# Performance work log

Measured on AMD Instinct MI355X. Metric: run time of the kernel, lower is better.

Reference implementation:

```python
import jax, jax.numpy as jnp
import numpy as np

NUM_HEADS = 16


def _rope(x_BHLd, freqs_cis):
    # x: [B,H,L,d], freqs_cis: [L, d//2, 2] (cos, sin)
    B, H, L, d = x_BHLd.shape
    xs = x_BHLd.reshape(B, H, L, d // 2, 2)
    fc = freqs_cis.reshape(1, 1, L, d // 2, 2)
    real = xs[..., 0] * fc[..., 0] - xs[..., 1] * fc[..., 1]
    imag = xs[..., 1] * fc[..., 0] + xs[..., 0] * fc[..., 1]
    return jnp.stack([real, imag], axis=-1).reshape(B, H, L, d)


def setup_inputs() -> dict:
    key = jax.random.key(0)
    k1, k2 = jax.random.split(key)
    B, L, D = 1, 4096, 1024
    d = D // NUM_HEADS
    x = jax.random.normal(k1, (B, L, D), dtype=jnp.float32)
    Wqkv = jax.random.normal(k2, (D, 3 * D), dtype=jnp.float32) * (D ** -0.5)
    bqkv = jnp.zeros((3 * D,), dtype=jnp.float32)
    # true rotary cos/sin table: [L, d//2, 2]
    base = 10000.0
    inv_freq = 1.0 / (base ** (jnp.arange(0, d, 2, dtype=jnp.float32) / d))  # [d//2]
    t = jnp.arange(L, dtype=jnp.float32)
    ang = jnp.outer(t, inv_freq)  # [L, d//2]
    freqs_cis = jnp.stack([jnp.cos(ang), jnp.sin(ang)], axis=-1)  # [L, d//2, 2]
    return {"x": x, "freqs_cis": freqs_cis, "Wqkv": Wqkv, "bqkv": bqkv}


def reference(x, freqs_cis, Wqkv, bqkv):
    B, L, D = x.shape
    H = NUM_HEADS
    d = D // H
    qkv = x @ Wqkv + bqkv  # [B,L,3D]
    q, k, v = jnp.split(qkv, 3, axis=-1)
    split = lambda t: t.reshape(B, L, H, d).transpose(0, 2, 1, 3)  # [B,H,L,d]
    q, k, v = split(q), split(k), split(v)
    q = _rope(q, freqs_cis)
    k = _rope(k, freqs_cis)
    scale = 1.0 / jnp.sqrt(jnp.asarray(d, dtype=q.dtype))
    scores = jnp.einsum('bhqd,bhkd->bhqk', q, k) * scale  # [B,H,L,L]
    causal = jnp.tril(jnp.ones((L, L), dtype=bool))
    scores = jnp.where(causal, scores, jnp.asarray(-jnp.inf, dtype=scores.dtype))
    probs = jax.nn.softmax(scores, axis=-1)
    out = jnp.einsum('bhqk,bhkd->bhqd', probs, v)  # [B,H,L,d]
    return out.transpose(0, 2, 1, 3).reshape(B, L, D)
```

## Files before the change

### kernel.cpp

```cpp
#include <hip/hip_runtime.h>

typedef short short8 __attribute__((ext_vector_type(8)));
typedef float f32x4 __attribute__((ext_vector_type(4)));
typedef unsigned short u16;
typedef unsigned short u16x4 __attribute__((ext_vector_type(4)));
typedef unsigned short u16x8 __attribute__((ext_vector_type(8)));

#define L_SEQ 4096
#define NHEAD 16
#define HDIM  64
#define DMODEL 1024
#define N3    3072
#define HL    (L_SEQ * HDIM)

__device__ __forceinline__ u16 f2bf(float f) {
  union { float f; unsigned u; } v; v.f = f;
  return (u16)((v.u + 0x7fffu + ((v.u >> 16) & 1u)) >> 16);
}

__device__ __forceinline__ unsigned cvt_pk_bf16(float lo, float hi) {
  unsigned r;
  asm("v_cvt_pk_bf16_f32 %0, %1, %2" : "=v"(r) : "v"(lo), "v"(hi));
  return r;
}

__device__ __forceinline__ void gl2lds16(const void* g, void* l) {
  __builtin_amdgcn_global_load_lds(
      (const __attribute__((address_space(1))) unsigned int*)g,
      (__attribute__((address_space(3))) unsigned int*)l, 16, 0, 0);
}

__device__ __forceinline__ float fexp2(float x) { return __builtin_amdgcn_exp2f(x); }

__global__ void cvt_fused_kernel(const float* __restrict__ x, u16* __restrict__ xb,
                                 const float* __restrict__ W, u16* __restrict__ Wt) {
  if (blockIdx.x < 2048) {
    int i = blockIdx.x * blockDim.x + threadIdx.x;
    const f32x4* p = (const f32x4*)x + (size_t)i * 2;
    f32x4 a = p[0], b = p[1];
    u16x8 o;
    o[0] = f2bf(a[0]); o[1] = f2bf(a[1]); o[2] = f2bf(a[2]); o[3] = f2bf(a[3]);
    o[4] = f2bf(b[0]); o[5] = f2bf(b[1]); o[6] = f2bf(b[2]); o[7] = f2bf(b[3]);
    ((u16x8*)xb)[i] = o;
  } else {
    __shared__ float t[64][65];
    int idx = blockIdx.x - 2048;
    int k0 = (idx & 15) * 64, n0 = (idx >> 4) * 64;
    int tr = threadIdx.x >> 4;
    int tc = (threadIdx.x & 15) * 4;
    for (int rr = tr; rr < 64; rr += 16) {
      f32x4 v = *(const f32x4*)&W[(size_t)(k0 + rr) * N3 + n0 + tc];
      t[rr][tc] = v[0]; t[rr][tc + 1] = v[1]; t[rr][tc + 2] = v[2]; t[rr][tc + 3] = v[3];
    }
    __syncthreads();
    for (int rr = tr; rr < 64; rr += 16) {
      u16x4 o;
      o[0] = f2bf(t[tc + 0][rr]); o[1] = f2bf(t[tc + 1][rr]);
      o[2] = f2bf(t[tc + 2][rr]); o[3] = f2bf(t[tc + 3][rr]);
      *(u16x4*)&Wt[(size_t)(n0 + rr) * DMODEL + k0 + tc] = o;
    }
  }
}

#define GBM 128
#define GBN 128
#define GBK 64

__global__ __launch_bounds__(256, 2) void gemm_qkv_kernel(
    const u16* __restrict__ xb, const u16* __restrict__ wt,
    const float* __restrict__ bias, const float* __restrict__ freqs,
    u16* __restrict__ Qb, u16* __restrict__ Kb, u16* __restrict__ Vt) {
  __shared__ u16 Asm[GBM * GBK];
  __shared__ u16 Bsm[GBN * GBK];
  const int tid = threadIdx.x, lane = tid & 63, wid = tid >> 6;
  const int lr = lane & 15, lh = lane >> 4;
  const int swz = (blockIdx.x % 8) * 96 + blockIdx.x / 8;
  const int bx = swz % (N3 / GBN), by = swz / (N3 / GBN);
  const int m0 = by * GBM, n0 = bx * GBN;
  const int wr = wid >> 1, wc = wid & 1;
  const char* xbB = (const char*)xb;
  const char* wtB = (const char*)wt;
  char* AsmB = (char*)Asm;
  char* BsmB = (char*)Bsm;

  int pbase[4]; size_t srcAoff[4], srcBoff[4];
#pragma unroll
  for (int i = 0; i < 4; i++) {
    int p = wid * 4096 + i * 1024 + lane * 16;
    int row = p >> 7, slot = (p & 127) >> 4;
    int sw = (slot ^ (row & 7)) * 16;
    pbase[i] = p;
    srcAoff[i] = (size_t)(m0 + row) * (DMODEL * 2) + sw;
    srcBoff[i] = (size_t)(n0 + row) * (DMODEL * 2) + sw;
  }

  int aoff[4][2], boff[4][2];
#pragma unroll
  for (int mi = 0; mi < 4; mi++) {
    int row = wr * 64 + mi * 16 + lr;
#pragma unroll
    for (int kc = 0; kc < 2; kc++)
      aoff[mi][kc] = row * 128 + ((kc * 64 + lh * 16) ^ ((row & 7) << 4));
  }
#pragma unroll
  for (int ni = 0; ni < 4; ni++) {
    int row = wc * 64 + ni * 16 + lr;
#pragma unroll
    for (int kc = 0; kc < 2; kc++)
      boff[ni][kc] = row * 128 + ((kc * 64 + lh * 16) ^ ((row & 7) << 4));
  }

  f32x4 acc[4][4] = {};

  for (int k0 = 0; k0 < DMODEL; k0 += GBK) {
    __syncthreads();
#pragma unroll
    for (int i = 0; i < 4; i++) {
      gl2lds16(xbB + srcAoff[i] + (size_t)k0 * 2, AsmB + pbase[i]);
      gl2lds16(wtB + srcBoff[i] + (size_t)k0 * 2, BsmB + pbase[i]);
    }
    __syncthreads();
#pragma unroll
    for (int kc = 0; kc < 2; kc++) {
      short8 a[4], b[4];
#pragma unroll
      for (int mi = 0; mi < 4; mi++) a[mi] = *(const short8*)(AsmB + aoff[mi][kc]);
#pragma unroll
      for (int ni = 0; ni < 4; ni++) b[ni] = *(const short8*)(BsmB + boff[ni][kc]);
#pragma unroll
      for (int mi = 0; mi < 4; mi++)
#pragma unroll
        for (int ni = 0; ni < 4; ni++)
          acc[mi][ni] = __builtin_amdgcn_mfma_f32_16x16x32_bf16(a[mi], b[ni], acc[mi][ni], 0, 0, 0);
    }
  }

  const float QSCALE = 0.125f * 1.44269504088896f;
  const int colbase = n0 + wc * 64;
#pragma unroll
  for (int ni = 0; ni < 4; ni++) {
    int col = colbase + ni * 16 + lr;
    float bv = bias[col];
    int sect = col >> 10;
    int cc = col & 1023;
    int h = cc >> 6, j = cc & 63;
#pragma unroll
    for (int mi = 0; mi < 4; mi++) {
      int row0 = m0 + wr * 64 + mi * 16 + lh * 4;
      float v[4];
#pragma unroll
      for (int r = 0; r < 4; r++) v[r] = acc[mi][ni][r] + bv;
      if (sect < 2) {
        int i2 = j >> 1;
        bool odd = (j & 1) != 0;
#pragma unroll
        for (int r = 0; r < 4; r++) {
          float pv = __shfl_xor(v[r], 1);
          float2 cs = *(const float2*)&freqs[((size_t)(row0 + r) * 32 + i2) * 2];
          v[r] = odd ? (v[r] * cs.x + pv * cs.y) : (v[r] * cs.x - pv * cs.y);
          if (sect == 0) v[r] *= QSCALE;
        }
        u16* dst = (sect == 0 ? Qb : Kb) + (size_t)h * HL + (size_t)row0 * HDIM + j;
#pragma unroll
        for (int r = 0; r < 4; r++) dst[(size_t)r * HDIM] = f2bf(v[r]);
      } else {
        u16x4 o;
#pragma unroll
        for (int r = 0; r < 4; r++) o[r] = f2bf(v[r]);
        *(u16x4*)&Vt[(size_t)h * HL + (size_t)j * L_SEQ + row0] = o;
      }
    }
  }
}

#define QBLK 64
#define KBLK 64

__global__ __launch_bounds__(256, 4) void flash_kernel(
    const u16* __restrict__ Qb, const u16* __restrict__ Kb,
    const u16* __restrict__ Vt, float* __restrict__ out) {
  __shared__ char Ksm[2][KBLK * 128];
  __shared__ char Vsm[2][HDIM * KBLK * 2];
  __shared__ char Psm[4][16 * 128];
  const int tid = threadIdx.x, lane = tid & 63, wid = tid >> 6;
  const int lr = lane & 15, lh = lane >> 4;
  const int bid = blockIdx.x;
  const int h = bid & 15;
  const int pr = bid >> 4;
  const char* Qh = (const char*)(Qb + (size_t)h * HL);
  const char* Kh = (const char*)(Kb + (size_t)h * HL);
  const char* Vh = (const char*)(Vt + (size_t)h * HL);
  char* Pw = Psm[wid];

  int pOff[2], KsrcOff[2], VsrcOff[2];
#pragma unroll
  for (int i = 0; i < 2; i++) {
    int p = wid * 2048 + i * 1024 + lane * 16;
    int row = p >> 7, slot = (p & 127) >> 4;
    int sw = (slot ^ (row & 7)) << 4;
    pOff[i] = p;
    KsrcOff[i] = row * 128 + sw;
    VsrcOff[i] = row * (L_SEQ * 2) + sw;
  }

  for (int pass = 0; pass < 2; ++pass) {
    const int qb = pass == 0 ? (63 - pr) : pr;
    const int q0 = qb * QBLK;
    const int wmin = q0 + wid * 16;
    const int qrow = wmin + lr;
    const int nt = qb + 1;

    short8 qa[2];
    {
      int row = q0 + wid * 16 + lr;
#pragma unroll
      for (int kc = 0; kc < 2; kc++)
        qa[kc] = *(const short8*)(Qh + (size_t)row * 128 + kc * 64 + lh * 16);
    }

    f32x4 o[4] = {};
    float m_r = -__builtin_inff(), ls = 0.f;

#pragma unroll
    for (int i = 0; i < 2; i++) {
      gl2lds16(Kh + KsrcOff[i], Ksm[0] + pOff[i]);
      gl2lds16(Vh + VsrcOff[i], Vsm[0] + pOff[i]);
    }
    __syncthreads();

    for (int t = 0; t < nt; ++t) {
      const int kt = t * KBLK;
      const int cur = t & 1;
      if (t + 1 < nt) {
        const size_t kn128 = (size_t)(kt + KBLK) * 128;
        const size_t kn2 = (size_t)(kt + KBLK) * 2;
#pragma unroll
        for (int i = 0; i < 2; i++) {
          gl2lds16(Kh + kn128 + KsrcOff[i], Ksm[cur ^ 1] + pOff[i]);
          gl2lds16(Vh + kn2 + VsrcOff[i], Vsm[cur ^ 1] + pOff[i]);
        }
      }
      const char* Kc = Ksm[cur];
      const char* Vc = Vsm[cur];

      f32x4 sfr[4];
      __builtin_amdgcn_s_setprio(1);
#pragma unroll
      for (int ni = 0; ni < 4; ni++) {
        int row = ni * 16 + lr;
        short8 bk0 = *(const short8*)(Kc + row * 128 + ((lh * 16) ^ ((row & 7) << 4)));
        short8 bk1 = *(const short8*)(Kc + row * 128 + ((64 + lh * 16) ^ ((row & 7) << 4)));
        f32x4 z = {};
        z = __builtin_amdgcn_mfma_f32_16x16x32_bf16(bk0, qa[0], z, 0, 0, 0);
        z = __builtin_amdgcn_mfma_f32_16x16x32_bf16(bk1, qa[1], z, 0, 0, 0);
        sfr[ni] = z;
      }
      __builtin_amdgcn_s_setprio(0);

      if (kt + KBLK - 1 > wmin) {
#pragma unroll
        for (int ni = 0; ni < 4; ni++)
#pragma unroll
          for (int r = 0; r < 4; r++)
            if (kt + ni * 16 + lh * 4 + r > qrow) sfr[ni][r] = -__builtin_inff();
      }

      float pmax = sfr[0][0];
#pragma unroll
      for (int ni = 0; ni < 4; ni++)
#pragma unroll
        for (int r = 0; r < 4; r++) pmax = fmaxf(pmax, sfr[ni][r]);
      pmax = fmaxf(pmax, __shfl_xor(pmax, 16));
      pmax = fmaxf(pmax, __shfl_xor(pmax, 32));

      if (__any(pmax > m_r + 8.f)) {
        float mn = fmaxf(m_r, pmax);
        float alpha = fexp2(m_r - mn);
        m_r = mn;
        ls *= alpha;
        float ao[4];
#pragma unroll
        for (int r = 0; r < 4; r++) ao[r] = __shfl(alpha, (lane & 48) | (lh * 4 + r));
#pragma unroll
        for (int vn = 0; vn < 4; vn++)
#pragma unroll
          for (int r = 0; r < 4; r++) o[vn][r] *= ao[r];
      }

      float psum = 0.f;
      unsigned Wp[4][2];
#pragma unroll
      for (int ni = 0; ni < 4; ni++) {
        float p0 = fexp2(sfr[ni][0] - m_r);
        float p1 = fexp2(sfr[ni][1] - m_r);
        float p2 = fexp2(sfr[ni][2] - m_r);
        float p3 = fexp2(sfr[ni][3] - m_r);
        psum += (p0 + p1) + (p2 + p3);
        Wp[ni][0] = cvt_pk_bf16(p0, p1);
        Wp[ni][1] = cvt_pk_bf16(p2, p3);
      }
      ls += psum;

#pragma unroll
      for (int ni = 0; ni < 4; ni++) {
        uint2 w2; w2.x = Wp[ni][0]; w2.y = Wp[ni][1];
        *(uint2*)(Pw + lr * 128 + ((ni * 32 + lh * 8) ^ ((lr & 7) << 4))) = w2;
      }
      asm volatile("s_waitcnt lgkmcnt(0)" ::: "memory");

      __builtin_amdgcn_s_setprio(1);
#pragma unroll
      for (int pc = 0; pc < 2; pc++) {
        short8 pa = *(const short8*)(Pw + lr * 128 + ((pc * 64 + lh * 16) ^ ((lr & 7) << 4)));
#pragma unroll
        for (int vn = 0; vn < 4; vn++) {
          int vrow = vn * 16 + lr;
          short8 bv = *(const short8*)(Vc + vrow * 128 + ((pc * 64 + lh * 16) ^ ((vrow & 7) << 4)));
          o[vn] = __builtin_amdgcn_mfma_f32_16x16x32_bf16(pa, bv, o[vn], 0, 0, 0);
        }
      }
      __builtin_amdgcn_s_setprio(0);

      __syncthreads();
    }

    ls += __shfl_xor(ls, 16);
    ls += __shfl_xor(ls, 32);
    float inv = 1.0f / ls;
    float invo[4];
#pragma unroll
    for (int r = 0; r < 4; r++) invo[r] = __shfl(inv, (lane & 48) | (lh * 4 + r));
#pragma unroll
    for (int r = 0; r < 4; r++) {
      int rowv = wmin + lh * 4 + r;
      float* op = out + (size_t)rowv * DMODEL + h * HDIM;
#pragma unroll
      for (int vn = 0; vn < 4; vn++) op[vn * 16 + lr] = o[vn][r] * invo[r];
    }
  }
}

extern "C" void kernel_launch(void* const* d_in, const int* in_sizes, int n_in,
                              void* d_out, int out_size, void* d_ws, size_t ws_size,
                              hipStream_t stream) {
  const float* x = (const float*)d_in[0];
  const float* freqs = (const float*)d_in[1];
  const float* W = (const float*)d_in[2];
  const float* bias = (const float*)d_in[3];
  float* out = (float*)d_out;

  char* ws = (char*)d_ws;
  u16* xb = (u16*)ws;
  u16* wt = (u16*)(ws + 8u * 1024 * 1024);
  u16* Qb = (u16*)(ws + 14u * 1024 * 1024);
  u16* Kb = (u16*)(ws + 22u * 1024 * 1024);
  u16* Vt = (u16*)(ws + 30u * 1024 * 1024);

  cvt_fused_kernel<<<2816, 256, 0, stream>>>(x, xb, W, wt);
  gemm_qkv_kernel<<<768, 256, 0, stream>>>(xb, wt, bias, freqs, Qb, Kb, Vt);
  flash_kernel<<<512, 256, 0, stream>>>(Qb, Kb, Vt, out);
}
```

Before: 129.4 us.

## Switch flash attention to 32x32 MFMA tiles with 128-row query blocks

```diff
diff --git a/kernel.cpp b/kernel.cpp
--- a/kernel.cpp
+++ b/kernel.cpp
@@ -2,6 +2,7 @@
 
 typedef short short8 __attribute__((ext_vector_type(8)));
 typedef float f32x4 __attribute__((ext_vector_type(4)));
+typedef float f32x16 __attribute__((ext_vector_type(16)));
 typedef unsigned short u16;
 typedef unsigned short u16x4 __attribute__((ext_vector_type(4)));
 typedef unsigned short u16x8 __attribute__((ext_vector_type(8)));
@@ -173,24 +174,34 @@
   }
 }
 
-#define QBLK 64
+#define QBLK 128
 #define KBLK 64
-
-__global__ __launch_bounds__(256, 4) void flash_kernel(
+#define LD8(p) (*(const short8*)(p))
+
+__global__ __launch_bounds__(256, 2) void flash_kernel(
     const u16* __restrict__ Qb, const u16* __restrict__ Kb,
     const u16* __restrict__ Vt, float* __restrict__ out) {
   __shared__ char Ksm[2][KBLK * 128];
   __shared__ char Vsm[2][HDIM * KBLK * 2];
-  __shared__ char Psm[4][16 * 128];
   const int tid = threadIdx.x, lane = tid & 63, wid = tid >> 6;
-  const int lr = lane & 15, lh = lane >> 4;
+  const int l31 = lane & 31, hf = lane >> 5;
   const int bid = blockIdx.x;
   const int h = bid & 15;
-  const int pr = bid >> 4;
+  const int qt = 31 - (bid >> 4);
+  const int q0 = qt * QBLK;
+  const int q0w = q0 + wid * 32;
+  const int qrow = q0w + l31;
   const char* Qh = (const char*)(Qb + (size_t)h * HL);
   const char* Kh = (const char*)(Kb + (size_t)h * HL);
   const char* Vh = (const char*)(Vt + (size_t)h * HL);
-  char* Pw = Psm[wid];
+
+  short8 qa[4];
+#pragma unroll
+  for (int ds = 0; ds < 4; ds++)
+    qa[ds] = LD8(Qh + (size_t)qrow * 128 + ds * 32 + hf * 16);
+
+  f32x16 o0 = {}, o1 = {};
+  float m_r = -__builtin_inff(), ls = 0.f;
 
   int pOff[2], KsrcOff[2], VsrcOff[2];
 #pragma unroll
@@ -203,74 +214,73 @@
     VsrcOff[i] = row * (L_SEQ * 2) + sw;
   }
 
-  for (int pass = 0; pass < 2; ++pass) {
-    const int qb = pass == 0 ? (63 - pr) : pr;
-    const int q0 = qb * QBLK;
-    const int wmin = q0 + wid * 16;
-    const int qrow = wmin + lr;
-    const int nt = qb + 1;
-
-    short8 qa[2];
-    {
-      int row = q0 + wid * 16 + lr;
-#pragma unroll
-      for (int kc = 0; kc < 2; kc++)
-        qa[kc] = *(const short8*)(Qh + (size_t)row * 128 + kc * 64 + lh * 16);
-    }
-
-    f32x4 o[4] = {};
-    float m_r = -__builtin_inff(), ls = 0.f;
-
-#pragma unroll
-    for (int i = 0; i < 2; i++) {
-      gl2lds16(Kh + KsrcOff[i], Ksm[0] + pOff[i]);
-      gl2lds16(Vh + VsrcOff[i], Vsm[0] + pOff[i]);
-    }
-    __syncthreads();
-
-    for (int t = 0; t < nt; ++t) {
-      const int kt = t * KBLK;
-      const int cur = t & 1;
-      if (t + 1 < nt) {
-        const size_t kn128 = (size_t)(kt + KBLK) * 128;
-        const size_t kn2 = (size_t)(kt + KBLK) * 2;
-#pragma unroll
-        for (int i = 0; i < 2; i++) {
-          gl2lds16(Kh + kn128 + KsrcOff[i], Ksm[cur ^ 1] + pOff[i]);
-          gl2lds16(Vh + kn2 + VsrcOff[i], Vsm[cur ^ 1] + pOff[i]);
+  const int nt = 2 * qt + 2;
+
+#pragma unroll
+  for (int i = 0; i < 2; i++) {
+    gl2lds16(Kh + KsrcOff[i], Ksm[0] + pOff[i]);
+    gl2lds16(Vh + VsrcOff[i], Vsm[0] + pOff[i]);
+  }
+  __syncthreads();
+
+  for (int t = 0; t < nt; ++t) {
+    const int kt = t * KBLK;
+    const int cur = t & 1;
+    if (t + 1 < nt) {
+      const size_t kn128 = (size_t)(kt + KBLK) * 128;
+      const size_t kn2 = (size_t)(kt + KBLK) * 2;
+#pragma unroll
+      for (int i = 0; i < 2; i++) {
+        gl2lds16(Kh + kn128 + KsrcOff[i], Ksm[cur ^ 1] + pOff[i]);
+        gl2lds16(Vh + kn2 + VsrcOff[i], Vsm[cur ^ 1] + pOff[i]);
+      }
+    }
+    const char* Kc = Ksm[cur];
+    const char* Vc = Vsm[cur];
+
+    if (kt <= q0w + 31) {
+      const bool do1 = (kt + 32) <= (q0w + 31);
+
+      f32x16 s0 = {}, s1 = {};
+      __builtin_amdgcn_s_setprio(1);
+#pragma unroll
+      for (int ds = 0; ds < 4; ds++) {
+        int off = (ds * 32 + hf * 16);
+        short8 k0 = LD8(Kc + l31 * 128 + (off ^ ((l31 & 7) << 4)));
+        s0 = __builtin_amdgcn_mfma_f32_32x32x16_bf16(k0, qa[ds], s0, 0, 0, 0);
+      }
+      if (do1) {
+#pragma unroll
+        for (int ds = 0; ds < 4; ds++) {
+          int off = (ds * 32 + hf * 16);
+          short8 k1 = LD8(Kc + (32 + l31) * 128 + (off ^ (((32 + l31) & 7) << 4)));
+          s1 = __builtin_amdgcn_mfma_f32_32x32x16_bf16(k1, qa[ds], s1, 0, 0, 0);
         }
       }
-      const char* Kc = Ksm[cur];
-      const char* Vc = Vsm[cur];
-
-      f32x4 sfr[4];
-      __builtin_amdgcn_s_setprio(1);
-#pragma unroll
-      for (int ni = 0; ni < 4; ni++) {
-        int row = ni * 16 + lr;
-        short8 bk0 = *(const short8*)(Kc + row * 128 + ((lh * 16) ^ ((row & 7) << 4)));
-        short8 bk1 = *(const short8*)(Kc + row * 128 + ((64 + lh * 16) ^ ((row & 7) << 4)));
-        f32x4 z = {};
-        z = __builtin_amdgcn_mfma_f32_16x16x32_bf16(bk0, qa[0], z, 0, 0, 0);
-        z = __builtin_amdgcn_mfma_f32_16x16x32_bf16(bk1, qa[1], z, 0, 0, 0);
-        sfr[ni] = z;
-      }
       __builtin_amdgcn_s_setprio(0);
 
-      if (kt + KBLK - 1 > wmin) {
-#pragma unroll
-        for (int ni = 0; ni < 4; ni++)
-#pragma unroll
-          for (int r = 0; r < 4; r++)
-            if (kt + ni * 16 + lh * 4 + r > qrow) sfr[ni][r] = -__builtin_inff();
-      }
-
-      float pmax = sfr[0][0];
-#pragma unroll
-      for (int ni = 0; ni < 4; ni++)
-#pragma unroll
-        for (int r = 0; r < 4; r++) pmax = fmaxf(pmax, sfr[ni][r]);
-      pmax = fmaxf(pmax, __shfl_xor(pmax, 16));
+      if (kt + 31 > q0w) {
+#pragma unroll
+        for (int r = 0; r < 16; r++) {
+          int kl = (r & 3) + 8 * (r >> 2) + 4 * hf;
+          if (kt + kl > qrow) s0[r] = -__builtin_inff();
+        }
+      }
+      if (do1 && (kt + 63 > q0w)) {
+#pragma unroll
+        for (int r = 0; r < 16; r++) {
+          int kl = (r & 3) + 8 * (r >> 2) + 4 * hf;
+          if (kt + 32 + kl > qrow) s1[r] = -__builtin_inff();
+        }
+      }
+
+      float pmax = s0[0];
+#pragma unroll
+      for (int r = 1; r < 16; r++) pmax = fmaxf(pmax, s0[r]);
+      if (do1) {
+#pragma unroll
+        for (int r = 0; r < 16; r++) pmax = fmaxf(pmax, s1[r]);
+      }
       pmax = fmaxf(pmax, __shfl_xor(pmax, 32));
 
       if (__any(pmax > m_r + 8.f)) {
@@ -278,65 +288,67 @@
         float alpha = fexp2(m_r - mn);
         m_r = mn;
         ls *= alpha;
-        float ao[4];
-#pragma unroll
-        for (int r = 0; r < 4; r++) ao[r] = __shfl(alpha, (lane & 48) | (lh * 4 + r));
-#pragma unroll
-        for (int vn = 0; vn < 4; vn++)
-#pragma unroll
-          for (int r = 0; r < 4; r++) o[vn][r] *= ao[r];
-      }
-
-      float psum = 0.f;
-      unsigned Wp[4][2];
-#pragma unroll
-      for (int ni = 0; ni < 4; ni++) {
-        float p0 = fexp2(sfr[ni][0] - m_r);
-        float p1 = fexp2(sfr[ni][1] - m_r);
-        float p2 = fexp2(sfr[ni][2] - m_r);
-        float p3 = fexp2(sfr[ni][3] - m_r);
-        psum += (p0 + p1) + (p2 + p3);
-        Wp[ni][0] = cvt_pk_bf16(p0, p1);
-        Wp[ni][1] = cvt_pk_bf16(p2, p3);
-      }
-      ls += psum;
-
-#pragma unroll
-      for (int ni = 0; ni < 4; ni++) {
-        uint2 w2; w2.x = Wp[ni][0]; w2.y = Wp[ni][1];
-        *(uint2*)(Pw + lr * 128 + ((ni * 32 + lh * 8) ^ ((lr & 7) << 4))) = w2;
-      }
-      asm volatile("s_waitcnt lgkmcnt(0)" ::: "memory");
-
-      __builtin_amdgcn_s_setprio(1);
-#pragma unroll
-      for (int pc = 0; pc < 2; pc++) {
-        short8 pa = *(const short8*)(Pw + lr * 128 + ((pc * 64 + lh * 16) ^ ((lr & 7) << 4)));
-#pragma unroll
-        for (int vn = 0; vn < 4; vn++) {
-          int vrow = vn * 16 + lr;
-          short8 bv = *(const short8*)(Vc + vrow * 128 + ((pc * 64 + lh * 16) ^ ((vrow & 7) << 4)));
-          o[vn] = __builtin_amdgcn_mfma_f32_16x16x32_bf16(pa, bv, o[vn], 0, 0, 0);
-        }
-      }
-      __builtin_amdgcn_s_setprio(0);
-
-      __syncthreads();
-    }
-
-    ls += __shfl_xor(ls, 16);
-    ls += __shfl_xor(ls, 32);
-    float inv = 1.0f / ls;
-    float invo[4];
-#pragma unroll
-    for (int r = 0; r < 4; r++) invo[r] = __shfl(inv, (lane & 48) | (lh * 4 + r));
-#pragma unroll
-    for (int r = 0; r < 4; r++) {
-      int rowv = wmin + lh * 4 + r;
-      float* op = out + (size_t)rowv * DMODEL + h * HDIM;
-#pragma unroll
-      for (int vn = 0; vn < 4; vn++) op[vn * 16 + lr] = o[vn][r] * invo[r];
-    }
+        float ao[16];
+#pragma unroll
+        for (int r = 0; r < 16; r++)
+          ao[r] = __shfl(alpha, (r & 3) + 8 * (r >> 2) + 4 * hf);
+#pragma unroll
+        for (int r = 0; r < 16; r++) { o0[r] *= ao[r]; o1[r] *= ao[r]; }
+      }
+
+#define KST_BLOCK(SREG, KST)                                                      \
+      {                                                                           \
+        float e[16]; float ps = 0.f;                                              \
+        _Pragma("unroll")                                                         \
+        for (int r = 0; r < 16; r++) { e[r] = fexp2(SREG[r] - m_r); ps += e[r]; } \
+        ls += ps;                                                                 \
+        unsigned pk[8];                                                           \
+        _Pragma("unroll")                                                         \
+        for (int m = 0; m < 8; m++) pk[m] = cvt_pk_bf16(e[2 * m], e[2 * m + 1]);  \
+        unsigned x0 = __shfl_xor(hf ? pk[0] : pk[2], 32);                         \
+        unsigned x1 = __shfl_xor(hf ? pk[1] : pk[3], 32);                         \
+        unsigned x2 = __shfl_xor(hf ? pk[4] : pk[6], 32);                         \
+        unsigned x3 = __shfl_xor(hf ? pk[5] : pk[7], 32);                         \
+        union { unsigned u[4]; short8 s8; } A0, A1;                               \
+        A0.u[0] = hf ? x0 : pk[0]; A0.u[1] = hf ? x1 : pk[1];                     \
+        A0.u[2] = hf ? pk[2] : x0; A0.u[3] = hf ? pk[3] : x1;                     \
+        A1.u[0] = hf ? x2 : pk[4]; A1.u[1] = hf ? x3 : pk[5];                     \
+        A1.u[2] = hf ? pk[6] : x2; A1.u[3] = hf ? pk[7] : x3;                     \
+        __builtin_amdgcn_s_setprio(1);                                            \
+        {                                                                         \
+          int vr0 = l31, vr1 = 32 + l31;                                          \
+          short8 v00 = LD8(Vc + vr0 * 128 + (((KST) * 64 + hf * 16) ^ ((vr0 & 7) << 4)));      \
+          short8 v01 = LD8(Vc + vr0 * 128 + (((KST) * 64 + 32 + hf * 16) ^ ((vr0 & 7) << 4))); \
+          o0 = __builtin_amdgcn_mfma_f32_32x32x16_bf16(A0.s8, v00, o0, 0, 0, 0);  \
+          o0 = __builtin_amdgcn_mfma_f32_32x32x16_bf16(A1.s8, v01, o0, 0, 0, 0);  \
+          short8 v10 = LD8(Vc + vr1 * 128 + (((KST) * 64 + hf * 16) ^ ((vr1 & 7) << 4)));      \
+          short8 v11 = LD8(Vc + vr1 * 128 + (((KST) * 64 + 32 + hf * 16) ^ ((vr1 & 7) << 4))); \
+          o1 = __builtin_amdgcn_mfma_f32_32x32x16_bf16(A0.s8, v10, o1, 0, 0, 0);  \
+          o1 = __builtin_amdgcn_mfma_f32_32x32x16_bf16(A1.s8, v11, o1, 0, 0, 0);  \
+        }                                                                         \
+        __builtin_amdgcn_s_setprio(0);                                            \
+      }
+
+      KST_BLOCK(s0, 0)
+      if (do1) KST_BLOCK(s1, 1)
+#undef KST_BLOCK
+    }
+
+    __syncthreads();
+  }
+
+  ls += __shfl_xor(ls, 32);
+  float inv = 1.0f / ls;
+  float invo[16];
+#pragma unroll
+  for (int r = 0; r < 16; r++)
+    invo[r] = __shfl(inv, (r & 3) + 8 * (r >> 2) + 4 * hf);
+#pragma unroll
+  for (int r = 0; r < 16; r++) {
+    int rowq = q0w + (r & 3) + 8 * (r >> 2) + 4 * hf;
+    float* op = out + (size_t)rowq * DMODEL + h * HDIM;
+    op[l31] = o0[r] * invo[r];
+    op[32 + l31] = o1[r] * invo[r];
   }
 }
 
```

After: 145.0 us. 12.0% more time.

## Use 128-row query tiles with 8 waves sharing each K/V tile

Applied to the files above, without the earlier changes.

```diff
diff --git a/kernel.cpp b/kernel.cpp
--- a/kernel.cpp
+++ b/kernel.cpp
@@ -173,76 +173,65 @@
   }
 }
 
-#define QBLK 64
+#define QBLK 128
 #define KBLK 64
 
-__global__ __launch_bounds__(256, 4) void flash_kernel(
+__global__ __launch_bounds__(512, 2) void flash_kernel(
     const u16* __restrict__ Qb, const u16* __restrict__ Kb,
     const u16* __restrict__ Vt, float* __restrict__ out) {
   __shared__ char Ksm[2][KBLK * 128];
   __shared__ char Vsm[2][HDIM * KBLK * 2];
-  __shared__ char Psm[4][16 * 128];
+  __shared__ char Psm[8][16 * 128];
   const int tid = threadIdx.x, lane = tid & 63, wid = tid >> 6;
   const int lr = lane & 15, lh = lane >> 4;
   const int bid = blockIdx.x;
   const int h = bid & 15;
-  const int pr = bid >> 4;
+  const int s = bid >> 4;
+  const int qt = (s < 16) ? s : (47 - s);
+  const int q0 = qt * QBLK;
   const char* Qh = (const char*)(Qb + (size_t)h * HL);
   const char* Kh = (const char*)(Kb + (size_t)h * HL);
   const char* Vh = (const char*)(Vt + (size_t)h * HL);
+
+  const int wmin = q0 + wid * 16;
+  const int qrow = wmin + lr;
   char* Pw = Psm[wid];
 
-  int pOff[2], KsrcOff[2], VsrcOff[2];
-#pragma unroll
-  for (int i = 0; i < 2; i++) {
-    int p = wid * 2048 + i * 1024 + lane * 16;
+  short8 qa[2];
+#pragma unroll
+  for (int kc = 0; kc < 2; kc++)
+    qa[kc] = *(const short8*)(Qh + (size_t)qrow * 128 + kc * 64 + lh * 16);
+
+  f32x4 o[4] = {};
+  float m_r = -__builtin_inff(), ls = 0.f;
+
+  int pOff, KsrcOff, VsrcOff;
+  {
+    int p = wid * 1024 + lane * 16;
     int row = p >> 7, slot = (p & 127) >> 4;
     int sw = (slot ^ (row & 7)) << 4;
-    pOff[i] = p;
-    KsrcOff[i] = row * 128 + sw;
-    VsrcOff[i] = row * (L_SEQ * 2) + sw;
-  }
-
-  for (int pass = 0; pass < 2; ++pass) {
-    const int qb = pass == 0 ? (63 - pr) : pr;
-    const int q0 = qb * QBLK;
-    const int wmin = q0 + wid * 16;
-    const int qrow = wmin + lr;
-    const int nt = qb + 1;
-
-    short8 qa[2];
-    {
-      int row = q0 + wid * 16 + lr;
-#pragma unroll
-      for (int kc = 0; kc < 2; kc++)
-        qa[kc] = *(const short8*)(Qh + (size_t)row * 128 + kc * 64 + lh * 16);
-    }
-
-    f32x4 o[4] = {};
-    float m_r = -__builtin_inff(), ls = 0.f;
-
-#pragma unroll
-    for (int i = 0; i < 2; i++) {
-      gl2lds16(Kh + KsrcOff[i], Ksm[0] + pOff[i]);
-      gl2lds16(Vh + VsrcOff[i], Vsm[0] + pOff[i]);
-    }
-    __syncthreads();
-
-    for (int t = 0; t < nt; ++t) {
-      const int kt = t * KBLK;
-      const int cur = t & 1;
-      if (t + 1 < nt) {
-        const size_t kn128 = (size_t)(kt + KBLK) * 128;
-        const size_t kn2 = (size_t)(kt + KBLK) * 2;
-#pragma unroll
-        for (int i = 0; i < 2; i++) {
-          gl2lds16(Kh + kn128 + KsrcOff[i], Ksm[cur ^ 1] + pOff[i]);
-          gl2lds16(Vh + kn2 + VsrcOff[i], Vsm[cur ^ 1] + pOff[i]);
-        }
-      }
-      const char* Kc = Ksm[cur];
-      const char* Vc = Vsm[cur];
-
+    pOff = p;
+    KsrcOff = row * 128 + sw;
+    VsrcOff = row * (L_SEQ * 2) + sw;
+  }
+
+  const int nt = 2 * qt + 2;
+
+  gl2lds16(Kh + KsrcOff, Ksm[0] + pOff);
+  gl2lds16(Vh + VsrcOff, Vsm[0] + pOff);
+  __syncthreads();
+
+  for (int t = 0; t < nt; ++t) {
+    const int kt = t * KBLK;
+    const int cur = t & 1;
+    if (t + 1 < nt) {
+      gl2lds16(Kh + (size_t)(kt + KBLK) * 128 + KsrcOff, Ksm[cur ^ 1] + pOff);
+      gl2lds16(Vh + (size_t)(kt + KBLK) * 2 + VsrcOff, Vsm[cur ^ 1] + pOff);
+    }
+    const char* Kc = Ksm[cur];
+    const char* Vc = Vsm[cur];
+
+    if (kt <= wmin + 15) {
       f32x4 sfr[4];
       __builtin_amdgcn_s_setprio(1);
 #pragma unroll
@@ -320,23 +309,23 @@
         }
       }
       __builtin_amdgcn_s_setprio(0);
-
-      __syncthreads();
-    }
-
-    ls += __shfl_xor(ls, 16);
-    ls += __shfl_xor(ls, 32);
-    float inv = 1.0f / ls;
-    float invo[4];
-#pragma unroll
-    for (int r = 0; r < 4; r++) invo[r] = __shfl(inv, (lane & 48) | (lh * 4 + r));
-#pragma unroll
-    for (int r = 0; r < 4; r++) {
-      int rowv = wmin + lh * 4 + r;
-      float* op = out + (size_t)rowv * DMODEL + h * HDIM;
-#pragma unroll
-      for (int vn = 0; vn < 4; vn++) op[vn * 16 + lr] = o[vn][r] * invo[r];
-    }
+    }
+
+    __syncthreads();
+  }
+
+  ls += __shfl_xor(ls, 16);
+  ls += __shfl_xor(ls, 32);
+  float inv = 1.0f / ls;
+  float invo[4];
+#pragma unroll
+  for (int r = 0; r < 4; r++) invo[r] = __shfl(inv, (lane & 48) | (lh * 4 + r));
+#pragma unroll
+  for (int r = 0; r < 4; r++) {
+    int rowv = wmin + lh * 4 + r;
+    float* op = out + (size_t)rowv * DMODEL + h * HDIM;
+#pragma unroll
+    for (int vn = 0; vn < 4; vn++) op[vn * 16 + lr] = o[vn][r] * invo[r];
   }
 }
 
@@ -358,5 +347,5 @@
 
   cvt_fused_kernel<<<2816, 256, 0, stream>>>(x, xb, W, wt);
   gemm_qkv_kernel<<<768, 256, 0, stream>>>(xb, wt, bias, freqs, Qb, Kb, Vt);
-  flash_kernel<<<512, 256, 0, stream>>>(Qb, Kb, Vt, out);
-}
+  flash_kernel<<<512, 512, 0, stream>>>(Qb, Kb, Vt, out);
+}
```

Result: slower. 135.5 us (+4.7%).

## Double KV tile to 128 keys and skip fully masked causal sub-tiles

Applied to the files above, without the earlier changes.

```diff
diff --git a/kernel.cpp b/kernel.cpp
--- a/kernel.cpp
+++ b/kernel.cpp
@@ -174,14 +174,14 @@
 }
 
 #define QBLK 64
-#define KBLK 64
-
-__global__ __launch_bounds__(256, 4) void flash_kernel(
+#define KBLK 128
+
+__global__ __launch_bounds__(256, 2) void flash_kernel(
     const u16* __restrict__ Qb, const u16* __restrict__ Kb,
     const u16* __restrict__ Vt, float* __restrict__ out) {
   __shared__ char Ksm[2][KBLK * 128];
   __shared__ char Vsm[2][HDIM * KBLK * 2];
-  __shared__ char Psm[4][16 * 128];
+  __shared__ char Psm[4][16 * 256];
   const int tid = threadIdx.x, lane = tid & 63, wid = tid >> 6;
   const int lr = lane & 15, lh = lane >> 4;
   const int bid = blockIdx.x;
@@ -192,15 +192,19 @@
   const char* Vh = (const char*)(Vt + (size_t)h * HL);
   char* Pw = Psm[wid];
 
-  int pOff[2], KsrcOff[2], VsrcOff[2];
-#pragma unroll
-  for (int i = 0; i < 2; i++) {
-    int p = wid * 2048 + i * 1024 + lane * 16;
-    int row = p >> 7, slot = (p & 127) >> 4;
-    int sw = (slot ^ (row & 7)) << 4;
+  int pOff[4], KsrcOff[4], VsrcOff[4];
+#pragma unroll
+  for (int i = 0; i < 4; i++) {
+    int p = wid * 4096 + i * 1024 + lane * 16;
+    {
+      int row = p >> 7, slot = (p & 127) >> 4;
+      KsrcOff[i] = row * 128 + ((slot ^ (row & 7)) << 4);
+    }
+    {
+      int row = p >> 8, slot = (p & 255) >> 4;
+      VsrcOff[i] = row * (L_SEQ * 2) + ((slot ^ (row & 7)) << 4);
+    }
     pOff[i] = p;
-    KsrcOff[i] = row * 128 + sw;
-    VsrcOff[i] = row * (L_SEQ * 2) + sw;
   }
 
   for (int pass = 0; pass < 2; ++pass) {
@@ -208,21 +212,18 @@
     const int q0 = qb * QBLK;
     const int wmin = q0 + wid * 16;
     const int qrow = wmin + lr;
-    const int nt = qb + 1;
+    const int nt = qb / 2 + 1;
 
     short8 qa[2];
-    {
-      int row = q0 + wid * 16 + lr;
-#pragma unroll
-      for (int kc = 0; kc < 2; kc++)
-        qa[kc] = *(const short8*)(Qh + (size_t)row * 128 + kc * 64 + lh * 16);
-    }
+#pragma unroll
+    for (int kc = 0; kc < 2; kc++)
+      qa[kc] = *(const short8*)(Qh + (size_t)qrow * 128 + kc * 64 + lh * 16);
 
     f32x4 o[4] = {};
     float m_r = -__builtin_inff(), ls = 0.f;
 
 #pragma unroll
-    for (int i = 0; i < 2; i++) {
+    for (int i = 0; i < 4; i++) {
       gl2lds16(Kh + KsrcOff[i], Ksm[0] + pOff[i]);
       gl2lds16(Vh + VsrcOff[i], Vsm[0] + pOff[i]);
     }
@@ -235,41 +236,44 @@
         const size_t kn128 = (size_t)(kt + KBLK) * 128;
         const size_t kn2 = (size_t)(kt + KBLK) * 2;
 #pragma unroll
-        for (int i = 0; i < 2; i++) {
+        for (int i = 0; i < 4; i++) {
           gl2lds16(Kh + kn128 + KsrcOff[i], Ksm[cur ^ 1] + pOff[i]);
           gl2lds16(Vh + kn2 + VsrcOff[i], Vsm[cur ^ 1] + pOff[i]);
         }
       }
       const char* Kc = Ksm[cur];
       const char* Vc = Vsm[cur];
-
-      f32x4 sfr[4];
+      const bool need_mask = (kt + KBLK - 1) > wmin;
+
+      f32x4 sfr[8];
+      float pmax = -__builtin_inff();
       __builtin_amdgcn_s_setprio(1);
 #pragma unroll
-      for (int ni = 0; ni < 4; ni++) {
-        int row = ni * 16 + lr;
-        short8 bk0 = *(const short8*)(Kc + row * 128 + ((lh * 16) ^ ((row & 7) << 4)));
-        short8 bk1 = *(const short8*)(Kc + row * 128 + ((64 + lh * 16) ^ ((row & 7) << 4)));
-        f32x4 z = {};
-        z = __builtin_amdgcn_mfma_f32_16x16x32_bf16(bk0, qa[0], z, 0, 0, 0);
-        z = __builtin_amdgcn_mfma_f32_16x16x32_bf16(bk1, qa[1], z, 0, 0, 0);
-        sfr[ni] = z;
+      for (int ni = 0; ni < 8; ni++) {
+        if (kt + ni * 16 <= wmin + 15) {
+          int row = ni * 16 + lr;
+          short8 bk0 = *(const short8*)(Kc + row * 128 + ((lh * 16) ^ ((row & 7) << 4)));
+          short8 bk1 = *(const short8*)(Kc + row * 128 + ((64 + lh * 16) ^ ((row & 7) << 4)));
+          f32x4 z = {};
+          z = __builtin_amdgcn_mfma_f32_16x16x32_bf16(bk0, qa[0], z, 0, 0, 0);
+          z = __builtin_amdgcn_mfma_f32_16x16x32_bf16(bk1, qa[1], z, 0, 0, 0);
+          sfr[ni] = z;
+        }
       }
       __builtin_amdgcn_s_setprio(0);
 
-      if (kt + KBLK - 1 > wmin) {
-#pragma unroll
-        for (int ni = 0; ni < 4; ni++)
-#pragma unroll
-          for (int r = 0; r < 4; r++)
-            if (kt + ni * 16 + lh * 4 + r > qrow) sfr[ni][r] = -__builtin_inff();
-      }
-
-      float pmax = sfr[0][0];
-#pragma unroll
-      for (int ni = 0; ni < 4; ni++)
-#pragma unroll
-        for (int r = 0; r < 4; r++) pmax = fmaxf(pmax, sfr[ni][r]);
+#pragma unroll
+      for (int ni = 0; ni < 8; ni++) {
+        if (kt + ni * 16 <= wmin + 15) {
+          if (need_mask) {
+#pragma unroll
+            for (int r = 0; r < 4; r++)
+              if (kt + ni * 16 + lh * 4 + r > qrow) sfr[ni][r] = -__builtin_inff();
+          }
+#pragma unroll
+          for (int r = 0; r < 4; r++) pmax = fmaxf(pmax, sfr[ni][r]);
+        }
+      }
       pmax = fmaxf(pmax, __shfl_xor(pmax, 16));
       pmax = fmaxf(pmax, __shfl_xor(pmax, 32));
 
@@ -288,35 +292,36 @@
       }
 
       float psum = 0.f;
-      unsigned Wp[4][2];
-#pragma unroll
-      for (int ni = 0; ni < 4; ni++) {
-        float p0 = fexp2(sfr[ni][0] - m_r);
-        float p1 = fexp2(sfr[ni][1] - m_r);
-        float p2 = fexp2(sfr[ni][2] - m_r);
-        float p3 = fexp2(sfr[ni][3] - m_r);
-        psum += (p0 + p1) + (p2 + p3);
-        Wp[ni][0] = cvt_pk_bf16(p0, p1);
-        Wp[ni][1] = cvt_pk_bf16(p2, p3);
+#pragma unroll
+      for (int ni = 0; ni < 8; ni++) {
+        uint2 w2;
+        if (kt + ni * 16 <= wmin + 15) {
+          float p0 = fexp2(sfr[ni][0] - m_r);
+          float p1 = fexp2(sfr[ni][1] - m_r);
+          float p2 = fexp2(sfr[ni][2] - m_r);
+          float p3 = fexp2(sfr[ni][3] - m_r);
+          psum += (p0 + p1) + (p2 + p3);
+          w2.x = cvt_pk_bf16(p0, p1);
+          w2.y = cvt_pk_bf16(p2, p3);
+        } else {
+          w2.x = 0u; w2.y = 0u;
+        }
+        *(uint2*)(Pw + lr * 256 + ((ni * 32 + lh * 8) ^ ((lr & 7) << 4))) = w2;
       }
       ls += psum;
-
-#pragma unroll
-      for (int ni = 0; ni < 4; ni++) {
-        uint2 w2; w2.x = Wp[ni][0]; w2.y = Wp[ni][1];
-        *(uint2*)(Pw + lr * 128 + ((ni * 32 + lh * 8) ^ ((lr & 7) << 4))) = w2;
-      }
       asm volatile("s_waitcnt lgkmcnt(0)" ::: "memory");
 
       __builtin_amdgcn_s_setprio(1);
 #pragma unroll
-      for (int pc = 0; pc < 2; pc++) {
-        short8 pa = *(const short8*)(Pw + lr * 128 + ((pc * 64 + lh * 16) ^ ((lr & 7) << 4)));
-#pragma unroll
-        for (int vn = 0; vn < 4; vn++) {
-          int vrow = vn * 16 + lr;
-          short8 bv = *(const short8*)(Vc + vrow * 128 + ((pc * 64 + lh * 16) ^ ((vrow & 7) << 4)));
-          o[vn] = __builtin_amdgcn_mfma_f32_16x16x32_bf16(pa, bv, o[vn], 0, 0, 0);
+      for (int pc = 0; pc < 4; pc++) {
+        if (kt + pc * 32 <= wmin + 15) {
+          short8 pa = *(const short8*)(Pw + lr * 256 + ((pc * 64 + lh * 16) ^ ((lr & 7) << 4)));
+#pragma unroll
+          for (int vn = 0; vn < 4; vn++) {
+            int vrow = vn * 16 + lr;
+            short8 bv = *(const short8*)(Vc + vrow * 256 + ((pc * 64 + lh * 16) ^ ((vrow & 7) << 4)));
+            o[vn] = __builtin_amdgcn_mfma_f32_16x16x32_bf16(pa, bv, o[vn], 0, 0, 0);
+          }
         }
       }
       __builtin_amdgcn_s_setprio(0);
```

Measured after the change: 139.6 us. +7.9%, slower.
